# Optimization experiments

Hardware: AMD Instinct MI355X
Metric: run time of the kernel (lower is better)

## Reference

```python
import jax, jax.numpy as jnp
import numpy as np

B_SZ, T, H, N, L = 4, 512, 256, 64, 4
EPS = 1e-5

def _hippo(n):
    i = np.arange(n)[:, None]; j = np.arange(n)[None, :]
    A = np.where(i >= j, ((-1.0) ** (i - j)) * np.sqrt((2 * i + 1.0) * (2 * j + 1.0)), 0.0)
    # scale to be contractive so the 512-step dense recurrence stays finite
    A = A / (1.1 * np.linalg.norm(A, 2))
    return A.astype(np.float32)

def _xavier(key, shape):
    fan_in, fan_out = shape[1], shape[0]
    a = float(np.sqrt(6.0 / (fan_in + fan_out)))
    return jax.random.uniform(key, shape, jnp.float32, -a, a)

def setup_inputs() -> dict:
    key = jax.random.key(0)
    ks = jax.random.split(key, 8)
    x = jax.random.normal(ks[0], (B_SZ, T, H), jnp.float32)
    A = jnp.broadcast_to(jnp.asarray(_hippo(N)), (L, N, N))
    Bm = jnp.stack([_xavier(jax.random.fold_in(ks[1], l), (N, H)) for l in range(L)])
    Cm = jnp.stack([_xavier(jax.random.fold_in(ks[2], l), (H, N)) for l in range(L)])
    Dm = jnp.stack([_xavier(jax.random.fold_in(ks[3], l), (H, H)) for l in range(L)])
    Win = _xavier(ks[4], (H, H)); bin_ = jnp.zeros((H,), jnp.float32)
    Wout = _xavier(ks[5], (H, H)); bout = jnp.zeros((H,), jnp.float32)
    return {"x": x, "Win": Win, "bin_": bin_, "Wout": Wout, "bout": bout,
            "A": A, "Bm": Bm, "Cm": Cm, "Dm": Dm}

def _ln(x):
    m = jnp.mean(x, -1, keepdims=True)
    v = jnp.mean((x - m) ** 2, -1, keepdims=True)
    return (x - m) / jnp.sqrt(v + EPS)

def _ssm_layer(h, A, B, C, D):
    # h: (B,T,H); dense state (B,N,H)
    Cbar = C.mean(0)            # mean over output rows (matches C_state.mean(dim=2))
    BT = B.T                    # (H,N)
    DT = D.T                    # (H,H)
    def step(state, u):        # state (B,N,H), u (B,H)
        y = jnp.einsum('bnh,n->bh', state, Cbar) + u @ DT   # output uses pre-update state
        new_state = jnp.einsum('nm,bmh->bnh', A, state) + (u @ BT)[:, :, None]
        return new_state, y
    state0 = jnp.zeros((h.shape[0], A.shape[0], h.shape[2]), h.dtype)
    _, ys = jax.lax.scan(step, state0, jnp.swapaxes(h, 0, 1))  # scan over T
    y = jnp.swapaxes(ys, 0, 1)
    y = jax.nn.gelu(y, approximate=False) + h   # GELU -> (dropout=0) -> residual
    return _ln(y)

def reference(x, Win, bin_, Wout, bout, A, Bm, Cm, Dm):
    h = x @ Win.T + bin_
    for l in range(L):
        h = _ssm_layer(h, A[l], Bm[l], Cm[l], Dm[l])
    h = _ln(h)
    return h @ Wout.T + bout
```

## Files before the change

kernel.cpp:

```cpp
#include <hip/hip_runtime.h>

#define TSEQ 512
#define HDIM 256
#define NDIM 64
#define LC   48
#define YSTR 260
#define NWB  128

typedef __attribute__((ext_vector_type(4))) float  f32x4;
typedef __attribute__((ext_vector_type(8))) short  s16x8;
typedef __attribute__((ext_vector_type(4))) unsigned short u16x4;
typedef unsigned long long u64;
typedef unsigned short us;

#define MFMA16 __builtin_amdgcn_mfma_f32_16x16x32_bf16

__device__ __forceinline__ float wave_red(float v) {
#pragma unroll
    for (int m = 1; m < 64; m <<= 1) v += __shfl_xor(v, m, 64);
    return v;
}
__device__ __forceinline__ float lane_bcast(float v, int l) {
    return __int_as_float(__builtin_amdgcn_readlane(__float_as_int(v), l));
}
__device__ __forceinline__ us f2bf(float f) {
    unsigned u = __float_as_uint(f);
    u += 0x7fffu + ((u >> 16) & 1u);
    return (us)(u >> 16);
}
__device__ __forceinline__ float bf2f(us h) {
    return __uint_as_float(((unsigned)h) << 16);
}
__device__ __forceinline__ int swz(int row, int chunk) {
    return row * 512 + (((chunk) ^ (row & 7)) << 4);
}

__device__ __forceinline__ void st_mall(float* p, float v) {
    __hip_atomic_store(p, v, __ATOMIC_RELAXED, __HIP_MEMORY_SCOPE_AGENT);
}
__device__ __forceinline__ u64 ld_mall8(const u64* p) {
    return __hip_atomic_load(p, __ATOMIC_RELAXED, __HIP_MEMORY_SCOPE_AGENT);
}
__device__ __forceinline__ void flag_set(unsigned* f) {
    __hip_atomic_store(f, 1u, __ATOMIC_RELAXED, __HIP_MEMORY_SCOPE_AGENT);
}
__device__ __forceinline__ void flag_wait(const unsigned* f) {
    while (__hip_atomic_load(f, __ATOMIC_RELAXED, __HIP_MEMORY_SCOPE_AGENT) == 0u)
        __builtin_amdgcn_s_sleep(1);
}

__global__ void __launch_bounds__(256) k_prep(
    const float* __restrict__ Win, const float* __restrict__ Wout,
    const float* __restrict__ Bm, const float* __restrict__ Dm,
    const float* __restrict__ Cm, const float* __restrict__ A,
    us* __restrict__ Win_bf, us* __restrict__ Wout_bf,
    us* __restrict__ Bm_bf, us* __restrict__ Dm_bf,
    float* __restrict__ cbar_g, float* __restrict__ wA8,
    unsigned* __restrict__ flags)
{
    __shared__ __align__(16) float Pa[4096];
    __shared__ __align__(16) float Pb[4096];
    const int gid = blockIdx.x, tid = threadIdx.x;

    if (gid < 128) {
        for (int q = gid * 256 + tid; q < 114688; q += 32768) {
            const float* s; us* d; int off;
            if (q < 16384)      { s = Win;  d = Win_bf;  off = q; }
            else if (q < 32768) { s = Wout; d = Wout_bf; off = q - 16384; }
            else if (q < 49152) { s = Bm;   d = Bm_bf;   off = q - 32768; }
            else                { s = Dm;   d = Dm_bf;   off = q - 49152; }
            f32x4 v = ((const f32x4*)s)[off];
            u16x4 p; p[0] = f2bf(v[0]); p[1] = f2bf(v[1]); p[2] = f2bf(v[2]); p[3] = f2bf(v[3]);
            ((u16x4*)d)[off] = p;
        }
        return;
    }
    if (gid == 128) {
        for (int i = tid; i < 4 + 4 * NWB; i += 256)
            __hip_atomic_store(&flags[i], 0u, __ATOMIC_RELAXED, __HIP_MEMORY_SCOPE_AGENT);
        const int l = tid >> 6, n = tid & 63;
        const float* cp = Cm + (size_t)l * HDIM * NDIM + n;
        float s0 = 0.f, s1 = 0.f, s2 = 0.f, s3 = 0.f;
        for (int h = 0; h < HDIM; h += 4) {
            s0 += cp[(h + 0) * NDIM]; s1 += cp[(h + 1) * NDIM];
            s2 += cp[(h + 2) * NDIM]; s3 += cp[(h + 3) * NDIM];
        }
        cbar_g[tid] = ((s0 + s1) + (s2 + s3)) * (1.0f / HDIM);
        return;
    }
    for (int q = tid; q < 1024; q += 256) ((f32x4*)Pa)[q] = ((const f32x4*)A)[q];
    __syncthreads();
    const int r0 = (tid >> 3) * 2, c0 = (tid & 7) * 8;
    const f32x4 z4 = {0.f, 0.f, 0.f, 0.f};
#pragma unroll 1
    for (int it = 0; it < 3; ++it) {
        const float* S = (it & 1) ? Pb : Pa;
        float*       D = (it & 1) ? Pa : Pb;
        f32x4 s00 = z4, s01 = z4, s10 = z4, s11 = z4;
        for (int k = 0; k < 64; ++k) {
            float a0 = S[r0 * 64 + k], a1 = S[(r0 + 1) * 64 + k];
            f32x4 b0 = *(const f32x4*)(S + k * 64 + c0);
            f32x4 b1 = *(const f32x4*)(S + k * 64 + c0 + 4);
            s00 += a0 * b0; s01 += a0 * b1; s10 += a1 * b0; s11 += a1 * b1;
        }
        *(f32x4*)(D + r0 * 64 + c0) = s00;       *(f32x4*)(D + r0 * 64 + c0 + 4) = s01;
        *(f32x4*)(D + (r0 + 1) * 64 + c0) = s10; *(f32x4*)(D + (r0 + 1) * 64 + c0 + 4) = s11;
        __syncthreads();
    }
    for (int q = tid; q < 1024; q += 256) ((f32x4*)wA8)[q] = ((const f32x4*)Pb)[q];
}

__global__ void __launch_bounds__(512, 2) k_fused(
    const float* __restrict__ x, const float* __restrict__ bin,
    const float* __restrict__ bout, const float* __restrict__ A,
    const float* __restrict__ wA8, const float* __restrict__ cbar_g,
    const us* __restrict__ Win_bf, const us* __restrict__ Wout_bf,
    const us* __restrict__ Bm_bf, const us* __restrict__ Dm_bf,
    float* __restrict__ wbuf, float* __restrict__ BiA, float* __restrict__ BiB,
    unsigned* __restrict__ flags, float* __restrict__ out)
{
    __shared__ __align__(16) char smem[53568];
    us*    xl   = (us*)smem;
    float* yl   = (float*)(smem + 8192);
    float* bwin = (float*)(smem + 24832);
    float* wlds = (float*)(smem + 41216);
    float* cfin = (float*)(smem + 53504);

    const int gid = blockIdx.x, tid = threadIdx.x;
    const int lane = tid & 63, wv = tid >> 6;
    const int m = lane & 15, cgq = lane >> 4;
    const f32x4 z4 = {0.f, 0.f, 0.f, 0.f};

    if (gid == NWB) {
        float* As  = (float*)smem;
        float* A8s = (float*)(smem + 16384);
        float* uls = (float*)(smem + 32768);
        for (int q = tid; q < 1024; q += 512) {
            ((f32x4*)As)[q]  = ((const f32x4*)A)[q];
            ((f32x4*)A8s)[q] = ((const f32x4*)wA8)[q];
        }
        __syncthreads();
        if (wv < 4) {
            const int l = wv;
            float u = cbar_g[l * 64 + lane];
            uls[(l * 8 + 0) * 64 + lane] = u;
#pragma unroll 1
            for (int s = 1; s < 8; ++s) {
                float p0 = 0.f, p1 = 0.f, p2 = 0.f, p3 = 0.f;
#pragma unroll
                for (int k = 0; k < 64; k += 4) {
                    p0 += As[(k + 0) * 64 + lane] * lane_bcast(u, k + 0);
                    p1 += As[(k + 1) * 64 + lane] * lane_bcast(u, k + 1);
                    p2 += As[(k + 2) * 64 + lane] * lane_bcast(u, k + 2);
                    p3 += As[(k + 3) * 64 + lane] * lane_bcast(u, k + 3);
                }
                u = (p0 + p1) + (p2 + p3);
                uls[(l * 8 + s) * 64 + lane] = u;
            }
        }
        __syncthreads();
        {
            const int p = wv;
            float u0 = uls[(0 * 8 + p) * 64 + lane];
            float u1 = uls[(1 * 8 + p) * 64 + lane];
            float u2 = uls[(2 * 8 + p) * 64 + lane];
            float u3 = uls[(3 * 8 + p) * 64 + lane];
#pragma unroll 1
            for (int k6 = 0; k6 < 6; ++k6) {
                const int j = p + 8 * k6;
                st_mall(&wbuf[(0 * LC + j) * 64 + lane], u0);
                st_mall(&wbuf[(1 * LC + j) * 64 + lane], u1);
                st_mall(&wbuf[(2 * LC + j) * 64 + lane], u2);
                st_mall(&wbuf[(3 * LC + j) * 64 + lane], u3);
                if (k6 < 5) {
                    float n0 = 0.f, n1 = 0.f, n2 = 0.f, n3 = 0.f;
#pragma unroll
                    for (int k = 0; k < 64; ++k) {
                        float a = A8s[k * 64 + lane];
                        n0 += a * lane_bcast(u0, k); n1 += a * lane_bcast(u1, k);
                        n2 += a * lane_bcast(u2, k); n3 += a * lane_bcast(u3, k);
                    }
                    u0 = n0; u1 = n1; u2 = n2; u3 = n3;
                }
            }
        }
        __syncthreads();
        if (tid < 4) flag_set(&flags[tid]);
        return;
    }

    const int b = gid >> 5, tb = gid & 31, t0 = tb * 16;
    const size_t grow = (size_t)(b * TSEQ + t0);

    {
        const f32x4* gs = (const f32x4*)(x + grow * HDIM);
#pragma unroll
        for (int k = 0; k < 2; ++k) {
            int q = tid + k * 512;
            int row = q >> 6, c4 = q & 63;
            f32x4 v = gs[q];
            u16x4 pk; pk[0] = f2bf(v[0]); pk[1] = f2bf(v[1]); pk[2] = f2bf(v[2]); pk[3] = f2bf(v[3]);
            *(u16x4*)((char*)xl + swz(row, c4 >> 1) + (c4 & 1) * 8) = pk;
        }
    }
    __syncthreads();

    {
        f32x4 accA = z4, accB = z4;
        const us* W0 = Win_bf + (size_t)(wv * 32 + m) * HDIM;
        const us* W1 = Win_bf + (size_t)(wv * 32 + 16 + m) * HDIM;
#pragma unroll
        for (int ks = 0; ks < 8; ++ks) {
            s16x8 av = *(const s16x8*)((const char*)xl + swz(m, ks * 4 + cgq));
            s16x8 b0 = *(const s16x8*)(W0 + ks * 32 + cgq * 8);
            s16x8 b1 = *(const s16x8*)(W1 + ks * 32 + cgq * 8);
            accA = MFMA16(av, b0, accA, 0, 0, 0);
            accB = MFMA16(av, b1, accB, 0, 0, 0);
        }
        __syncthreads();
        const int h0c = wv * 32 + m, h1c = wv * 32 + 16 + m;
        float bi0 = bin[h0c], bi1 = bin[h1c];
#pragma unroll
        for (int reg = 0; reg < 4; ++reg) {
            int trow = cgq * 4 + reg;
            *(us*)((char*)xl + swz(trow, h0c >> 3) + (h0c & 7) * 2) = f2bf(accA[reg] + bi0);
            *(us*)((char*)xl + swz(trow, h1c >> 3) + (h1c & 7) * 2) = f2bf(accB[reg] + bi1);
        }
    }
    __syncthreads();

    if (wv < 4) {
        f32x4 accb = z4;
        const us* B0 = Bm_bf + (size_t)(wv * 16 + m) * HDIM;
#pragma unroll
        for (int ks = 0; ks < 8; ++ks) {
            s16x8 av = *(const s16x8*)((const char*)xl + swz(m, ks * 4 + cgq));
            s16x8 bv = *(const s16x8*)(B0 + ks * 32 + cgq * 8);
            accb = MFMA16(av, bv, accb, 0, 0, 0);
        }
#pragma unroll
        for (int reg = 0; reg < 4; ++reg)
            st_mall(&BiA[(grow + cgq * 4 + reg) * NDIM + wv * 16 + m], accb[reg]);
    }
    __syncthreads();
    if (tid == 0) flag_set(&flags[4 + 0 * NWB + gid]);

#pragma unroll 1
    for (int l = 0; l < 4; ++l) {
        const us* Dl = Dm_bf + (size_t)l * HDIM * HDIM;
        const float* bi = (l & 1) ? BiB : BiA;
        float*       bo = (l & 1) ? BiA : BiB;

        f32x4 accA = z4, accB = z4;
        {
            const us* D0 = Dl + (size_t)(wv * 32 + m) * HDIM;
            const us* D1 = Dl + (size_t)(wv * 32 + 16 + m) * HDIM;
#pragma unroll
            for (int ks = 0; ks < 8; ++ks) {
                s16x8 av = *(const s16x8*)((const char*)xl + swz(m, ks * 4 + cgq));
                s16x8 b0 = *(const s16x8*)(D0 + ks * 32 + cgq * 8);
                s16x8 b1 = *(const s16x8*)(D1 + ks * 32 + cgq * 8);
                accA = MFMA16(av, b0, accA, 0, 0, 0);
                accB = MFMA16(av, b1, accB, 0, 0, 0);
            }
        }

        {
            const unsigned* fp = nullptr;
            if (lane == 3) fp = &flags[l];
            else if (lane < 3 && (tb - 1 - (int)lane) >= 0) fp = &flags[4 + l * NWB + gid - 1 - lane];
            if (fp) flag_wait(fp);
        }

        {
            const u64* ws8 = (const u64*)(wbuf + (size_t)l * LC * NDIM);
            for (int q = tid; q < LC * NDIM / 2; q += 512)
                ((u64*)wlds)[q] = ld_mall8(&ws8[q]);
            const u64* bi8 = (const u64*)(bi + (size_t)b * TSEQ * NDIM);
#pragma unroll
            for (int k = 0; k < 4; ++k) {
                int q = tid + k * 512;
                int r = q >> 5, cc = q & 31;
                int t = t0 - LC + r;
                ((u64*)bwin)[q] = (t >= 0) ? ld_mall8(&bi8[(size_t)t * 32 + cc]) : 0ull;
            }
        }
        __syncthreads();

        {
            const int r0 = wv * 2;
            float c0 = 0.f, c1 = 0.f;
            float v0 = bwin[(LC - 1 + r0) * NDIM + lane];
            float v1 = bwin[(LC + r0) * NDIM + lane];
#pragma unroll
            for (int j = 0; j < LC; ++j) {
                float wj = wlds[j * NDIM + lane];
                c0 += wj * v0; c1 += wj * v1;
                v1 = v0;
                int nr = LC - 2 + r0 - j; nr = nr < 0 ? 0 : nr;
                v0 = bwin[nr * NDIM + lane];
            }
            c0 = wave_red(c0); c1 = wave_red(c1);
            if (lane == 0) { cfin[r0] = c0; cfin[r0 + 1] = c1; }
        }
        __syncthreads();

#pragma unroll
        for (int nt = 0; nt < 2; ++nt) {
            int hcol = wv * 32 + nt * 16 + m;
#pragma unroll
            for (int reg = 0; reg < 4; ++reg) {
                int trow = cgq * 4 + reg;
                float val = (nt ? accB[reg] : accA[reg]) + cfin[trow];
                float g = 0.5f * val * (1.0f + erff(val * 0.70710678118654752f));
                float r = bf2f(*(const us*)((const char*)xl + swz(trow, hcol >> 3) + (hcol & 7) * 2));
                yl[trow * YSTR + hcol] = g + r;
            }
        }
        __syncthreads();

        {
            const bool last = (l == 3);
#pragma unroll
            for (int q = 0; q < 2; ++q) {
                int r = wv * 2 + q;
                f32x4 yv = *(const f32x4*)(yl + r * YSTR + lane * 4);
                float s = (yv[0] + yv[1]) + (yv[2] + yv[3]);
                float sq = yv[0] * yv[0] + yv[1] * yv[1] + yv[2] * yv[2] + yv[3] * yv[3];
                s = wave_red(s); sq = wave_red(sq);
                float mn = s * (1.0f / HDIM);
                float var = sq * (1.0f / HDIM) - mn * mn;
                float rs = rsqrtf(var + 1e-5f);
                if (last) { float vz = var * rs * rs; rs = rs * rsqrtf(vz + 1e-5f); }
                u16x4 zp;
                zp[0] = f2bf((yv[0] - mn) * rs); zp[1] = f2bf((yv[1] - mn) * rs);
                zp[2] = f2bf((yv[2] - mn) * rs); zp[3] = f2bf((yv[3] - mn) * rs);
                *(u16x4*)((char*)xl + swz(r, lane >> 1) + (lane & 1) * 8) = zp;
            }
        }
        __syncthreads();

        if (l < 3) {
            if (wv < 4) {
                f32x4 accb = z4;
                const us* B0 = Bm_bf + (size_t)(l + 1) * NDIM * HDIM + (size_t)(wv * 16 + m) * HDIM;
#pragma unroll
                for (int ks = 0; ks < 8; ++ks) {
                    s16x8 av = *(const s16x8*)((const char*)xl + swz(m, ks * 4 + cgq));
                    s16x8 bv = *(const s16x8*)(B0 + ks * 32 + cgq * 8);
                    accb = MFMA16(av, bv, accb, 0, 0, 0);
                }
#pragma unroll
                for (int reg = 0; reg < 4; ++reg)
                    st_mall(&bo[(grow + cgq * 4 + reg) * NDIM + wv * 16 + m], accb[reg]);
            }
            __syncthreads();
            if (tid == 0) flag_set(&flags[4 + (l + 1) * NWB + gid]);
        } else {
            f32x4 a2A = z4, a2B = z4;
            const us* W0 = Wout_bf + (size_t)(wv * 32 + m) * HDIM;
            const us* W1 = Wout_bf + (size_t)(wv * 32 + 16 + m) * HDIM;
#pragma unroll
            for (int ks = 0; ks < 8; ++ks) {
                s16x8 av = *(const s16x8*)((const char*)xl + swz(m, ks * 4 + cgq));
                s16x8 b0 = *(const s16x8*)(W0 + ks * 32 + cgq * 8);
                s16x8 b1 = *(const s16x8*)(W1 + ks * 32 + cgq * 8);
                a2A = MFMA16(av, b0, a2A, 0, 0, 0);
                a2B = MFMA16(av, b1, a2B, 0, 0, 0);
            }
#pragma unroll
            for (int nt = 0; nt < 2; ++nt) {
                int hcol = wv * 32 + nt * 16 + m;
                float bo2 = bout[hcol];
#pragma unroll
                for (int reg = 0; reg < 4; ++reg) {
                    int trow = cgq * 4 + reg;
                    out[(grow + trow) * HDIM + hcol] = (nt ? a2B[reg] : a2A[reg]) + bo2;
                }
            }
        }
    }
}

extern "C" void kernel_launch(void* const* d_in, const int* in_sizes, int n_in,
                              void* d_out, int out_size, void* d_ws, size_t ws_size,
                              hipStream_t stream) {
    (void)in_sizes; (void)n_in; (void)out_size; (void)ws_size;
    const float* x    = (const float*)d_in[0];
    const float* Win  = (const float*)d_in[1];
    const float* bin  = (const float*)d_in[2];
    const float* Wout = (const float*)d_in[3];
    const float* bout = (const float*)d_in[4];
    const float* A    = (const float*)d_in[5];
    const float* Bm   = (const float*)d_in[6];
    const float* Cm   = (const float*)d_in[7];
    const float* Dm   = (const float*)d_in[8];

    float* ws     = (float*)d_ws;
    float* wbuf   = ws;
    float* cbar_g = ws + 16384;
    float* wA8    = ws + 17408;
    float* biA    = ws + 21504;
    float* biB    = ws + 152576;
    unsigned* flags = (unsigned*)(ws + 283648);
    us* Win_bf  = (us*)(ws + 284672);
    us* Wout_bf = Win_bf + 65536;
    us* Bm_bf   = Wout_bf + 65536;
    us* Dm_bf   = Bm_bf + 65536;
    float* out  = (float*)d_out;

    k_prep<<<130, 256, 0, stream>>>(Win, Wout, Bm, Dm, Cm, A,
                                    Win_bf, Wout_bf, Bm_bf, Dm_bf, cbar_g, wA8, flags);
    k_fused<<<NWB + 1, 512, 0, stream>>>(x, bin, bout, A, wA8, cbar_g,
                                         Win_bf, Wout_bf, Bm_bf, Dm_bf,
                                         wbuf, biA, biB, flags, out);
}
```

Before: 71.94 us.

## Process two batch tiles per workgroup and compute LayerNorm stats in registers

Each worker workgroup now handles two 16-row tiles from different batches (b and b+2), halving the worker count to 64 and sharing weight fragment loads across both tiles in the MFMA loops. The LayerNorm is reworked to reduce per-row partial sums from MFMA accumulators via shuffles and a small LDS stats buffer, dropping the fp32 staging tile. The producer block publishes layer 0 kernel weights first with an early flag so layer 0 can start sooner. It trades parallelism across CUs and more register/LDS pressure for fewer redundant weight reads and better MFMA utilisation per block.

Measured after the change: 87.91 us. 22.2% more time.

```diff
diff --git a/kernel.cpp b/kernel.cpp
--- a/kernel.cpp
+++ b/kernel.cpp
@@ -4,8 +4,9 @@
 #define HDIM 256
 #define NDIM 64
 #define LC   48
-#define YSTR 260
-#define NWB  128
+#define MT   16
+#define NWB  64
+#define NTILE 128
 
 typedef __attribute__((ext_vector_type(4))) float  f32x4;
 typedef __attribute__((ext_vector_type(8))) short  s16x8;
@@ -15,11 +16,6 @@
 
 #define MFMA16 __builtin_amdgcn_mfma_f32_16x16x32_bf16
 
-__device__ __forceinline__ float wave_red(float v) {
-#pragma unroll
-    for (int m = 1; m < 64; m <<= 1) v += __shfl_xor(v, m, 64);
-    return v;
-}
 __device__ __forceinline__ float lane_bcast(float v, int l) {
     return __int_as_float(__builtin_amdgcn_readlane(__float_as_int(v), l));
 }
@@ -34,7 +30,6 @@
 __device__ __forceinline__ int swz(int row, int chunk) {
     return row * 512 + (((chunk) ^ (row & 7)) << 4);
 }
-
 __device__ __forceinline__ void st_mall(float* p, float v) {
     __hip_atomic_store(p, v, __ATOMIC_RELAXED, __HIP_MEMORY_SCOPE_AGENT);
 }
@@ -76,7 +71,7 @@
         return;
     }
     if (gid == 128) {
-        for (int i = tid; i < 4 + 4 * NWB; i += 256)
+        for (int i = tid; i < 4 + 4 * NTILE; i += 256)
             __hip_atomic_store(&flags[i], 0u, __ATOMIC_RELAXED, __HIP_MEMORY_SCOPE_AGENT);
         const int l = tid >> 6, n = tid & 63;
         const float* cp = Cm + (size_t)l * HDIM * NDIM + n;
@@ -119,12 +114,18 @@
     float* __restrict__ wbuf, float* __restrict__ BiA, float* __restrict__ BiB,
     unsigned* __restrict__ flags, float* __restrict__ out)
 {
-    __shared__ __align__(16) char smem[53568];
-    us*    xl   = (us*)smem;
-    float* yl   = (float*)(smem + 8192);
-    float* bwin = (float*)(smem + 24832);
-    float* wlds = (float*)(smem + 41216);
-    float* cfin = (float*)(smem + 53504);
+    __shared__ __align__(16) char smem[63616];
+    us*    xlA   = (us*)smem;
+    us*    xlB   = (us*)(smem + 8192);
+    float* bwinA = (float*)(smem + 16384);
+    float* bwinB = (float*)(smem + 32768);
+    float* wlds  = (float*)(smem + 49152);
+    float* cfinA = (float*)(smem + 61440);
+    float* cfinB = (float*)(smem + 61504);
+    float* pstat = (float*)(smem + 61568);
+    float* As  = (float*)smem;
+    float* A8s = (float*)(smem + 16384);
+    float* uls = (float*)(smem + 32768);
 
     const int gid = blockIdx.x, tid = threadIdx.x;
     const int lane = tid & 63, wv = tid >> 6;
@@ -132,18 +133,14 @@
     const f32x4 z4 = {0.f, 0.f, 0.f, 0.f};
 
     if (gid == NWB) {
-        float* As  = (float*)smem;
-        float* A8s = (float*)(smem + 16384);
-        float* uls = (float*)(smem + 32768);
         for (int q = tid; q < 1024; q += 512) {
             ((f32x4*)As)[q]  = ((const f32x4*)A)[q];
             ((f32x4*)A8s)[q] = ((const f32x4*)wA8)[q];
         }
         __syncthreads();
         if (wv < 4) {
-            const int l = wv;
-            float u = cbar_g[l * 64 + lane];
-            uls[(l * 8 + 0) * 64 + lane] = u;
+            float u = cbar_g[wv * 64 + lane];
+            uls[(wv * 8 + 0) * 64 + lane] = u;
 #pragma unroll 1
             for (int s = 1; s < 8; ++s) {
                 float p0 = 0.f, p1 = 0.f, p2 = 0.f, p3 = 0.f;
@@ -155,120 +152,155 @@
                     p3 += As[(k + 3) * 64 + lane] * lane_bcast(u, k + 3);
                 }
                 u = (p0 + p1) + (p2 + p3);
-                uls[(l * 8 + s) * 64 + lane] = u;
-            }
-        }
-        __syncthreads();
-        {
-            const int p = wv;
-            float u0 = uls[(0 * 8 + p) * 64 + lane];
-            float u1 = uls[(1 * 8 + p) * 64 + lane];
-            float u2 = uls[(2 * 8 + p) * 64 + lane];
-            float u3 = uls[(3 * 8 + p) * 64 + lane];
+                uls[(wv * 8 + s) * 64 + lane] = u;
+            }
+        }
+        __syncthreads();
+        {
+            float u = uls[wv * 64 + lane];
 #pragma unroll 1
             for (int k6 = 0; k6 < 6; ++k6) {
-                const int j = p + 8 * k6;
-                st_mall(&wbuf[(0 * LC + j) * 64 + lane], u0);
-                st_mall(&wbuf[(1 * LC + j) * 64 + lane], u1);
-                st_mall(&wbuf[(2 * LC + j) * 64 + lane], u2);
-                st_mall(&wbuf[(3 * LC + j) * 64 + lane], u3);
+                st_mall(&wbuf[(size_t)(wv + 8 * k6) * 64 + lane], u);
                 if (k6 < 5) {
-                    float n0 = 0.f, n1 = 0.f, n2 = 0.f, n3 = 0.f;
+                    float n0 = 0.f;
+#pragma unroll
+                    for (int k = 0; k < 64; ++k)
+                        n0 += A8s[k * 64 + lane] * lane_bcast(u, k);
+                    u = n0;
+                }
+            }
+        }
+        __syncthreads();
+        if (tid == 0) flag_set(&flags[0]);
+        {
+            float u1 = uls[(8 + wv) * 64 + lane];
+            float u2 = uls[(16 + wv) * 64 + lane];
+            float u3 = uls[(24 + wv) * 64 + lane];
+#pragma unroll 1
+            for (int k6 = 0; k6 < 6; ++k6) {
+                const int j = wv + 8 * k6;
+                st_mall(&wbuf[(size_t)(1 * LC + j) * 64 + lane], u1);
+                st_mall(&wbuf[(size_t)(2 * LC + j) * 64 + lane], u2);
+                st_mall(&wbuf[(size_t)(3 * LC + j) * 64 + lane], u3);
+                if (k6 < 5) {
+                    float n1 = 0.f, n2 = 0.f, n3 = 0.f;
 #pragma unroll
                     for (int k = 0; k < 64; ++k) {
                         float a = A8s[k * 64 + lane];
-                        n0 += a * lane_bcast(u0, k); n1 += a * lane_bcast(u1, k);
-                        n2 += a * lane_bcast(u2, k); n3 += a * lane_bcast(u3, k);
+                        n1 += a * lane_bcast(u1, k); n2 += a * lane_bcast(u2, k);
+                        n3 += a * lane_bcast(u3, k);
                     }
-                    u0 = n0; u1 = n1; u2 = n2; u3 = n3;
-                }
-            }
-        }
-        __syncthreads();
-        if (tid < 4) flag_set(&flags[tid]);
+                    u1 = n1; u2 = n2; u3 = n3;
+                }
+            }
+        }
+        __syncthreads();
+        if (tid < 3) flag_set(&flags[1 + tid]);
         return;
     }
 
-    const int b = gid >> 5, tb = gid & 31, t0 = tb * 16;
-    const size_t grow = (size_t)(b * TSEQ + t0);
+    const int bA = gid >> 5, tb = gid & 31, t0 = tb * MT;
+    const int bB = bA + 2;
+    const int tileA = bA * 32 + tb, tileB = bB * 32 + tb;
+    const size_t growA = (size_t)(bA * TSEQ + t0);
+    const size_t growB = (size_t)(bB * TSEQ + t0);
 
     {
-        const f32x4* gs = (const f32x4*)(x + grow * HDIM);
+        const f32x4* gsA = (const f32x4*)(x + growA * HDIM);
+        const f32x4* gsB = (const f32x4*)(x + growB * HDIM);
 #pragma unroll
         for (int k = 0; k < 2; ++k) {
             int q = tid + k * 512;
             int row = q >> 6, c4 = q & 63;
-            f32x4 v = gs[q];
+            f32x4 v = gsA[q];
             u16x4 pk; pk[0] = f2bf(v[0]); pk[1] = f2bf(v[1]); pk[2] = f2bf(v[2]); pk[3] = f2bf(v[3]);
-            *(u16x4*)((char*)xl + swz(row, c4 >> 1) + (c4 & 1) * 8) = pk;
+            *(u16x4*)((char*)xlA + swz(row, c4 >> 1) + (c4 & 1) * 8) = pk;
+            f32x4 w = gsB[q];
+            u16x4 pw; pw[0] = f2bf(w[0]); pw[1] = f2bf(w[1]); pw[2] = f2bf(w[2]); pw[3] = f2bf(w[3]);
+            *(u16x4*)((char*)xlB + swz(row, c4 >> 1) + (c4 & 1) * 8) = pw;
         }
     }
     __syncthreads();
 
     {
-        f32x4 accA = z4, accB = z4;
+        f32x4 hA0 = z4, hA1 = z4, hB0 = z4, hB1 = z4;
         const us* W0 = Win_bf + (size_t)(wv * 32 + m) * HDIM;
-        const us* W1 = Win_bf + (size_t)(wv * 32 + 16 + m) * HDIM;
+        const us* W1 = W0 + (size_t)16 * HDIM;
 #pragma unroll
         for (int ks = 0; ks < 8; ++ks) {
-            s16x8 av = *(const s16x8*)((const char*)xl + swz(m, ks * 4 + cgq));
-            s16x8 b0 = *(const s16x8*)(W0 + ks * 32 + cgq * 8);
-            s16x8 b1 = *(const s16x8*)(W1 + ks * 32 + cgq * 8);
-            accA = MFMA16(av, b0, accA, 0, 0, 0);
-            accB = MFMA16(av, b1, accB, 0, 0, 0);
-        }
-        __syncthreads();
-        const int h0c = wv * 32 + m, h1c = wv * 32 + 16 + m;
+            s16x8 avA = *(const s16x8*)((const char*)xlA + swz(m, ks * 4 + cgq));
+            s16x8 avB = *(const s16x8*)((const char*)xlB + swz(m, ks * 4 + cgq));
+            s16x8 w0 = *(const s16x8*)(W0 + ks * 32 + cgq * 8);
+            s16x8 w1 = *(const s16x8*)(W1 + ks * 32 + cgq * 8);
+            hA0 = MFMA16(avA, w0, hA0, 0, 0, 0);
+            hA1 = MFMA16(avA, w1, hA1, 0, 0, 0);
+            hB0 = MFMA16(avB, w0, hB0, 0, 0, 0);
+            hB1 = MFMA16(avB, w1, hB1, 0, 0, 0);
+        }
+        __syncthreads();
+        const int h0c = wv * 32 + m, h1c = h0c + 16;
         float bi0 = bin[h0c], bi1 = bin[h1c];
 #pragma unroll
         for (int reg = 0; reg < 4; ++reg) {
             int trow = cgq * 4 + reg;
-            *(us*)((char*)xl + swz(trow, h0c >> 3) + (h0c & 7) * 2) = f2bf(accA[reg] + bi0);
-            *(us*)((char*)xl + swz(trow, h1c >> 3) + (h1c & 7) * 2) = f2bf(accB[reg] + bi1);
+            *(us*)((char*)xlA + swz(trow, h0c >> 3) + (h0c & 7) * 2) = f2bf(hA0[reg] + bi0);
+            *(us*)((char*)xlA + swz(trow, h1c >> 3) + (h1c & 7) * 2) = f2bf(hA1[reg] + bi1);
+            *(us*)((char*)xlB + swz(trow, h0c >> 3) + (h0c & 7) * 2) = f2bf(hB0[reg] + bi0);
+            *(us*)((char*)xlB + swz(trow, h1c >> 3) + (h1c & 7) * 2) = f2bf(hB1[reg] + bi1);
         }
     }
     __syncthreads();
 
-    if (wv < 4) {
+    {
+        const int tw = (wv < 4) ? wv : wv - 4;
+        const us* xls = (wv < 4) ? xlA : xlB;
+        const size_t gr = (wv < 4) ? growA : growB;
         f32x4 accb = z4;
-        const us* B0 = Bm_bf + (size_t)(wv * 16 + m) * HDIM;
+        const us* B0 = Bm_bf + (size_t)(tw * 16 + m) * HDIM;
 #pragma unroll
         for (int ks = 0; ks < 8; ++ks) {
-            s16x8 av = *(const s16x8*)((const char*)xl + swz(m, ks * 4 + cgq));
+            s16x8 av = *(const s16x8*)((const char*)xls + swz(m, ks * 4 + cgq));
             s16x8 bv = *(const s16x8*)(B0 + ks * 32 + cgq * 8);
             accb = MFMA16(av, bv, accb, 0, 0, 0);
         }
 #pragma unroll
         for (int reg = 0; reg < 4; ++reg)
-            st_mall(&BiA[(grow + cgq * 4 + reg) * NDIM + wv * 16 + m], accb[reg]);
+            st_mall(&BiA[(gr + cgq * 4 + reg) * NDIM + tw * 16 + m], accb[reg]);
     }
     __syncthreads();
-    if (tid == 0) flag_set(&flags[4 + 0 * NWB + gid]);
+    if (tid == 0) flag_set(&flags[4 + 0 * NTILE + tileA]);
+    if (tid == 1) flag_set(&flags[4 + 0 * NTILE + tileB]);
 
 #pragma unroll 1
     for (int l = 0; l < 4; ++l) {
-        const us* Dl = Dm_bf + (size_t)l * HDIM * HDIM;
         const float* bi = (l & 1) ? BiB : BiA;
         float*       bo = (l & 1) ? BiA : BiB;
-
-        f32x4 accA = z4, accB = z4;
+        const us* Dl = Dm_bf + (size_t)l * HDIM * HDIM;
+
+        f32x4 dA0 = z4, dA1 = z4, dB0 = z4, dB1 = z4;
         {
             const us* D0 = Dl + (size_t)(wv * 32 + m) * HDIM;
-            const us* D1 = Dl + (size_t)(wv * 32 + 16 + m) * HDIM;
+            const us* D1 = D0 + (size_t)16 * HDIM;
 #pragma unroll
             for (int ks = 0; ks < 8; ++ks) {
-                s16x8 av = *(const s16x8*)((const char*)xl + swz(m, ks * 4 + cgq));
+                s16x8 avA = *(const s16x8*)((const char*)xlA + swz(m, ks * 4 + cgq));
+                s16x8 avB = *(const s16x8*)((const char*)xlB + swz(m, ks * 4 + cgq));
                 s16x8 b0 = *(const s16x8*)(D0 + ks * 32 + cgq * 8);
                 s16x8 b1 = *(const s16x8*)(D1 + ks * 32 + cgq * 8);
-                accA = MFMA16(av, b0, accA, 0, 0, 0);
-                accB = MFMA16(av, b1, accB, 0, 0, 0);
+                dA0 = MFMA16(avA, b0, dA0, 0, 0, 0);
+                dA1 = MFMA16(avA, b1, dA1, 0, 0, 0);
+                dB0 = MFMA16(avB, b0, dB0, 0, 0, 0);
+                dB1 = MFMA16(avB, b1, dB1, 0, 0, 0);
             }
         }
 
         {
             const unsigned* fp = nullptr;
             if (lane == 3) fp = &flags[l];
-            else if (lane < 3 && (tb - 1 - (int)lane) >= 0) fp = &flags[4 + l * NWB + gid - 1 - lane];
+            else if (lane < 3 && (tb - 1 - (int)lane) >= 0)
+                fp = &flags[4 + l * NTILE + tileA - 1 - lane];
+            else if (lane >= 4 && lane < 7 && (tb - 1 - (int)(lane - 4)) >= 0)
+                fp = &flags[4 + l * NTILE + tileB - 1 - (lane - 4)];
             if (fp) flag_wait(fp);
         }
 
@@ -276,45 +308,83 @@
             const u64* ws8 = (const u64*)(wbuf + (size_t)l * LC * NDIM);
             for (int q = tid; q < LC * NDIM / 2; q += 512)
                 ((u64*)wlds)[q] = ld_mall8(&ws8[q]);
-            const u64* bi8 = (const u64*)(bi + (size_t)b * TSEQ * NDIM);
+            const u64* biA8 = (const u64*)(bi + (size_t)bA * TSEQ * NDIM);
+            const u64* biB8 = (const u64*)(bi + (size_t)bB * TSEQ * NDIM);
 #pragma unroll
             for (int k = 0; k < 4; ++k) {
                 int q = tid + k * 512;
                 int r = q >> 5, cc = q & 31;
                 int t = t0 - LC + r;
-                ((u64*)bwin)[q] = (t >= 0) ? ld_mall8(&bi8[(size_t)t * 32 + cc]) : 0ull;
+                ((u64*)bwinA)[q] = (t >= 0) ? ld_mall8(&biA8[(size_t)t * 32 + cc]) : 0ull;
+                ((u64*)bwinB)[q] = (t >= 0) ? ld_mall8(&biB8[(size_t)t * 32 + cc]) : 0ull;
             }
         }
         __syncthreads();
 
         {
             const int r0 = wv * 2;
-            float c0 = 0.f, c1 = 0.f;
-            float v0 = bwin[(LC - 1 + r0) * NDIM + lane];
-            float v1 = bwin[(LC + r0) * NDIM + lane];
+            float cA0 = 0.f, cA1 = 0.f, cB0 = 0.f, cB1 = 0.f;
+            float vA0 = bwinA[(LC - 1 + r0) * NDIM + lane];
+            float vA1 = bwinA[(LC + r0) * NDIM + lane];
+            float vB0 = bwinB[(LC - 1 + r0) * NDIM + lane];
+            float vB1 = bwinB[(LC + r0) * NDIM + lane];
 #pragma unroll
             for (int j = 0; j < LC; ++j) {
                 float wj = wlds[j * NDIM + lane];
-                c0 += wj * v0; c1 += wj * v1;
-                v1 = v0;
+                cA0 += wj * vA0; cA1 += wj * vA1;
+                cB0 += wj * vB0; cB1 += wj * vB1;
+                vA1 = vA0; vB1 = vB0;
                 int nr = LC - 2 + r0 - j; nr = nr < 0 ? 0 : nr;
-                v0 = bwin[nr * NDIM + lane];
-            }
-            c0 = wave_red(c0); c1 = wave_red(c1);
-            if (lane == 0) { cfin[r0] = c0; cfin[r0 + 1] = c1; }
-        }
-        __syncthreads();
-
-#pragma unroll
-        for (int nt = 0; nt < 2; ++nt) {
-            int hcol = wv * 32 + nt * 16 + m;
+                vA0 = bwinA[nr * NDIM + lane];
+                vB0 = bwinB[nr * NDIM + lane];
+            }
+#pragma unroll
+            for (int k = 1; k < 64; k <<= 1) {
+                cA0 += __shfl_xor(cA0, k, 64); cA1 += __shfl_xor(cA1, k, 64);
+                cB0 += __shfl_xor(cB0, k, 64); cB1 += __shfl_xor(cB1, k, 64);
+            }
+            if (lane == 0) {
+                cfinA[r0] = cA0; cfinA[r0 + 1] = cA1;
+                cfinB[r0] = cB0; cfinB[r0 + 1] = cB1;
+            }
+        }
+        __syncthreads();
+
+        f32x4 oA0, oA1, oB0, oB1;
+        {
 #pragma unroll
             for (int reg = 0; reg < 4; ++reg) {
                 int trow = cgq * 4 + reg;
-                float val = (nt ? accB[reg] : accA[reg]) + cfin[trow];
-                float g = 0.5f * val * (1.0f + erff(val * 0.70710678118654752f));
-                float r = bf2f(*(const us*)((const char*)xl + swz(trow, hcol >> 3) + (hcol & 7) * 2));
-                yl[trow * YSTR + hcol] = g + r;
+                float cA = cfinA[trow], cB = cfinB[trow];
+                int c0 = wv * 32 + m, c1 = c0 + 16;
+                float v, g;
+                v = dA0[reg] + cA; g = 0.5f * v * (1.0f + erff(v * 0.70710678118654752f));
+                oA0[reg] = g + bf2f(*(const us*)((const char*)xlA + swz(trow, c0 >> 3) + (c0 & 7) * 2));
+                v = dA1[reg] + cA; g = 0.5f * v * (1.0f + erff(v * 0.70710678118654752f));
+                oA1[reg] = g + bf2f(*(const us*)((const char*)xlA + swz(trow, c1 >> 3) + (c1 & 7) * 2));
+                v = dB0[reg] + cB; g = 0.5f * v * (1.0f + erff(v * 0.70710678118654752f));
+                oB0[reg] = g + bf2f(*(const us*)((const char*)xlB + swz(trow, c0 >> 3) + (c0 & 7) * 2));
+                v = dB1[reg] + cB; g = 0.5f * v * (1.0f + erff(v * 0.70710678118654752f));
+                oB1[reg] = g + bf2f(*(const us*)((const char*)xlB + swz(trow, c1 >> 3) + (c1 & 7) * 2));
+            }
+#pragma unroll
+            for (int reg = 0; reg < 4; ++reg) {
+                float sA = oA0[reg] + oA1[reg];
+                float qA = oA0[reg] * oA0[reg] + oA1[reg] * oA1[reg];
+                float sB = oB0[reg] + oB1[reg];
+                float qB = oB0[reg] * oB0[reg] + oB1[reg] * oB1[reg];
+#pragma unroll
+                for (int k = 1; k < 16; k <<= 1) {
+                    sA += __shfl_xor(sA, k, 64); qA += __shfl_xor(qA, k, 64);
+                    sB += __shfl_xor(sB, k, 64); qB += __shfl_xor(qB, k, 64);
+                }
+                if (m == 0) {
+                    int row = cgq * 4 + reg;
+                    int ia = ((0 * 8 + wv) * 16 + row) * 2;
+                    int ib = ((1 * 8 + wv) * 16 + row) * 2;
+                    pstat[ia] = sA; pstat[ia + 1] = qA;
+                    pstat[ib] = sB; pstat[ib + 1] = qB;
+                }
             }
         }
         __syncthreads();
@@ -322,61 +392,79 @@
         {
             const bool last = (l == 3);
 #pragma unroll
-            for (int q = 0; q < 2; ++q) {
-                int r = wv * 2 + q;
-                f32x4 yv = *(const f32x4*)(yl + r * YSTR + lane * 4);
-                float s = (yv[0] + yv[1]) + (yv[2] + yv[3]);
-                float sq = yv[0] * yv[0] + yv[1] * yv[1] + yv[2] * yv[2] + yv[3] * yv[3];
-                s = wave_red(s); sq = wave_red(sq);
-                float mn = s * (1.0f / HDIM);
-                float var = sq * (1.0f / HDIM) - mn * mn;
-                float rs = rsqrtf(var + 1e-5f);
-                if (last) { float vz = var * rs * rs; rs = rs * rsqrtf(vz + 1e-5f); }
-                u16x4 zp;
-                zp[0] = f2bf((yv[0] - mn) * rs); zp[1] = f2bf((yv[1] - mn) * rs);
-                zp[2] = f2bf((yv[2] - mn) * rs); zp[3] = f2bf((yv[3] - mn) * rs);
-                *(u16x4*)((char*)xl + swz(r, lane >> 1) + (lane & 1) * 8) = zp;
+            for (int reg = 0; reg < 4; ++reg) {
+                int row = cgq * 4 + reg;
+                float sA = 0.f, qA = 0.f, sB = 0.f, qB = 0.f;
+#pragma unroll
+                for (int w = 0; w < 8; ++w) {
+                    sA += pstat[((0 * 8 + w) * 16 + row) * 2];
+                    qA += pstat[((0 * 8 + w) * 16 + row) * 2 + 1];
+                    sB += pstat[((1 * 8 + w) * 16 + row) * 2];
+                    qB += pstat[((1 * 8 + w) * 16 + row) * 2 + 1];
+                }
+                float mnA = sA * (1.0f / HDIM);
+                float varA = qA * (1.0f / HDIM) - mnA * mnA;
+                float rsA = rsqrtf(varA + 1e-5f);
+                float mnB = sB * (1.0f / HDIM);
+                float varB = qB * (1.0f / HDIM) - mnB * mnB;
+                float rsB = rsqrtf(varB + 1e-5f);
+                if (last) {
+                    float vzA = varA * rsA * rsA; rsA *= rsqrtf(vzA + 1e-5f);
+                    float vzB = varB * rsB * rsB; rsB *= rsqrtf(vzB + 1e-5f);
+                }
+                int c0 = wv * 32 + m, c1 = c0 + 16;
+                *(us*)((char*)xlA + swz(row, c0 >> 3) + (c0 & 7) * 2) = f2bf((oA0[reg] - mnA) * rsA);
+                *(us*)((char*)xlA + swz(row, c1 >> 3) + (c1 & 7) * 2) = f2bf((oA1[reg] - mnA) * rsA);
+                *(us*)((char*)xlB + swz(row, c0 >> 3) + (c0 & 7) * 2) = f2bf((oB0[reg] - mnB) * rsB);
+                *(us*)((char*)xlB + swz(row, c1 >> 3) + (c1 & 7) * 2) = f2bf((oB1[reg] - mnB) * rsB);
             }
         }
         __syncthreads();
 
         if (l < 3) {
-            if (wv < 4) {
+            {
+                const int tw = (wv < 4) ? wv : wv - 4;
+                const us* xls = (wv < 4) ? xlA : xlB;
+                const size_t gr = (wv < 4) ? growA : growB;
                 f32x4 accb = z4;
-                const us* B0 = Bm_bf + (size_t)(l + 1) * NDIM * HDIM + (size_t)(wv * 16 + m) * HDIM;
+                const us* B0 = Bm_bf + (size_t)(l + 1) * NDIM * HDIM + (size_t)(tw * 16 + m) * HDIM;
 #pragma unroll
                 for (int ks = 0; ks < 8; ++ks) {
-                    s16x8 av = *(const s16x8*)((const char*)xl + swz(m, ks * 4 + cgq));
+                    s16x8 av = *(const s16x8*)((const char*)xls + swz(m, ks * 4 + cgq));
                     s16x8 bv = *(const s16x8*)(B0 + ks * 32 + cgq * 8);
                     accb = MFMA16(av, bv, accb, 0, 0, 0);
                 }
 #pragma unroll
                 for (int reg = 0; reg < 4; ++reg)
-                    st_mall(&bo[(grow + cgq * 4 + reg) * NDIM + wv * 16 + m], accb[reg]);
+                    st_mall(&bo[(gr + cgq * 4 + reg) * NDIM + tw * 16 + m], accb[reg]);
             }
             __syncthreads();
-            if (tid == 0) flag_set(&flags[4 + (l + 1) * NWB + gid]);
+            if (tid == 0) flag_set(&flags[4 + (l + 1) * NTILE + tileA]);
+            if (tid == 1) flag_set(&flags[4 + (l + 1) * NTILE + tileB]);
         } else {
-            f32x4 a2A = z4, a2B = z4;
+            f32x4 qA0 = z4, qA1 = z4, qB0 = z4, qB1 = z4;
             const us* W0 = Wout_bf + (size_t)(wv * 32 + m) * HDIM;
-            const us* W1 = Wout_bf + (size_t)(wv * 32 + 16 + m) * HDIM;
+            const us* W1 = W0 + (size_t)16 * HDIM;
 #pragma unroll
             for (int ks = 0; ks < 8; ++ks) {
-                s16x8 av = *(const s16x8*)((const char*)xl + swz(m, ks * 4 + cgq));
-                s16x8 b0 = *(const s16x8*)(W0 + ks * 32 + cgq * 8);
-                s16x8 b1 = *(const s16x8*)(W1 + ks * 32 + cgq * 8);
-                a2A = MFMA16(av, b0, a2A, 0, 0, 0);
-                a2B = MFMA16(av, b1, a2B, 0, 0, 0);
-            }
-#pragma unroll
-            for (int nt = 0; nt < 2; ++nt) {
-                int hcol = wv * 32 + nt * 16 + m;
-                float bo2 = bout[hcol];
-#pragma unroll
-                for (int reg = 0; reg < 4; ++reg) {
-                    int trow = cgq * 4 + reg;
-                    out[(grow + trow) * HDIM + hcol] = (nt ? a2B[reg] : a2A[reg]) + bo2;
-                }
+                s16x8 avA = *(const s16x8*)((const char*)xlA + swz(m, ks * 4 + cgq));
+                s16x8 avB = *(const s16x8*)((const char*)xlB + swz(m, ks * 4 + cgq));
+                s16x8 w0 = *(const s16x8*)(W0 + ks * 32 + cgq * 8);
+                s16x8 w1 = *(const s16x8*)(W1 + ks * 32 + cgq * 8);
+                qA0 = MFMA16(avA, w0, qA0, 0, 0, 0);
+                qA1 = MFMA16(avA, w1, qA1, 0, 0, 0);
+                qB0 = MFMA16(avB, w0, qB0, 0, 0, 0);
+                qB1 = MFMA16(avB, w1, qB1, 0, 0, 0);
+            }
+            const int h0c = wv * 32 + m, h1c = h0c + 16;
+            float bo0 = bout[h0c], bo1 = bout[h1c];
+#pragma unroll
+            for (int reg = 0; reg < 4; ++reg) {
+                int trow = cgq * 4 + reg;
+                out[(growA + trow) * HDIM + h0c] = qA0[reg] + bo0;
+                out[(growA + trow) * HDIM + h1c] = qA1[reg] + bo1;
+                out[(growB + trow) * HDIM + h0c] = qB0[reg] + bo0;
+                out[(growB + trow) * HDIM + h1c] = qB1[reg] + bo1;
             }
         }
     }
```
